# Kernel optimization log

Measured on AMD Instinct MI355X. Metric: run time of the kernel, lower is better.

## Reference

```python
import jax, jax.numpy as jnp
import numpy as np

B, S, D_IN = 2, 2048, 1024
H, DH = 16, 64          # num_heads, hidden_size (per-head dim)
D_MODEL = H * DH        # 1024
D_OUT = DH * 8          # 512


def setup_inputs() -> dict:
    key = jax.random.key(0)
    ks = jax.random.split(key, 9)
    s_in = 1.0 / np.sqrt(D_IN)
    s_md = 1.0 / np.sqrt(D_MODEL)
    return {
        "x": jax.random.normal(ks[0], (B, S, D_IN), dtype=jnp.float32),
        "Wq": jax.random.uniform(ks[1], (D_IN, D_MODEL), jnp.float32, -s_in, s_in),
        "bq": jax.random.uniform(ks[2], (D_MODEL,), jnp.float32, -s_in, s_in),
        "Wk": jax.random.uniform(ks[3], (D_IN, D_MODEL), jnp.float32, -s_in, s_in),
        "bk": jax.random.uniform(ks[4], (D_MODEL,), jnp.float32, -s_in, s_in),
        "Wv": jax.random.uniform(ks[5], (D_IN, D_MODEL), jnp.float32, -s_in, s_in),
        "bv": jax.random.uniform(ks[6], (D_MODEL,), jnp.float32, -s_in, s_in),
        "Wo": jax.random.uniform(ks[7], (D_MODEL, D_OUT), jnp.float32, -s_md, s_md),
        "bo": jax.random.uniform(ks[8], (D_OUT,), jnp.float32, -s_md, s_md),
    }


def reference(x, Wq, bq, Wk, bk, Wv, bv, Wo, bo):
    b, s, _ = x.shape
    # QKV projections -> [B, H, S, DH]
    def proj(W, bias):
        y = jnp.einsum("bsd,de->bse", x, W) + bias
        return y.reshape(b, s, H, DH).transpose(0, 2, 1, 3)
    Q, K, V = proj(Wq, bq), proj(Wk, bk), proj(Wv, bv)
    scores = jnp.einsum("bhqd,bhkd->bhqk", Q, K) / jnp.sqrt(jnp.float32(DH))
    weights = jax.nn.softmax(scores, axis=-1)
    attn = jnp.einsum("bhqk,bhkd->bhqd", weights, V)  # [B, H, S, DH]
    attn = attn.transpose(0, 2, 1, 3).reshape(b, s, H * DH)
    return jnp.einsum("bsd,de->bse", attn, Wo) + bo
```

## Files before the change

### kernel.cpp

```cpp
#include <hip/hip_runtime.h>

typedef __attribute__((ext_vector_type(8))) __bf16 bf16x8;
typedef __attribute__((ext_vector_type(4))) __bf16 bf16x4;
typedef __attribute__((ext_vector_type(4))) float f32x4;

#define MFMA16x16x32(A, B, C) __builtin_amdgcn_mfma_f32_16x16x32_bf16(A, B, C, 0, 0, 0)

__device__ __forceinline__ unsigned short f2bf(float f) {
    unsigned int u = __float_as_uint(f);
    u += 0x7fffu + ((u >> 16) & 1u);
    return (unsigned short)(u >> 16);
}

__device__ __forceinline__ unsigned cvtpk_bf16(float lo, float hi) {
    unsigned r;
    asm("v_cvt_pk_bf16_f32 %0, %1, %2" : "=v"(r) : "v"(lo), "v"(hi));
    return r;
}

__device__ __forceinline__ float exp2_hw(float x) {
    float r;
    asm("v_exp_f32 %0, %1" : "=v"(r) : "v"(x));
    return r;
}

__device__ __forceinline__ void gload16(const void* src, void* lds) {
    __builtin_amdgcn_global_load_lds(
        (const __attribute__((address_space(1))) unsigned int*)src,
        (__attribute__((address_space(3))) unsigned int*)lds,
        16, 0, 0);
}

__global__ __launch_bounds__(256) void cvt_x_kernel(const float* __restrict__ x,
                                                    unsigned short* __restrict__ xb) {
    const int i = (blockIdx.x * 256 + threadIdx.x) * 4;
    const float4 v = *(const float4*)(x + i);
    ushort4 o;
    o.x = f2bf(v.x); o.y = f2bf(v.y); o.z = f2bf(v.z); o.w = f2bf(v.w);
    *(ushort4*)(xb + i) = o;
}

__global__ __launch_bounds__(256) void tr_w_all_kernel(
    const float* __restrict__ Wq, const float* __restrict__ Wk,
    const float* __restrict__ Wv, const float* __restrict__ Wo,
    unsigned short* __restrict__ Wqt, unsigned short* __restrict__ Wkt,
    unsigned short* __restrict__ Wvt, unsigned short* __restrict__ Wot)
{
    __shared__ float tile[32][33];
    int y = blockIdx.y;
    const float* W; unsigned short* Wt; int N;
    if (y < 32)      { W = Wq; Wt = Wqt; N = 1024; }
    else if (y < 64) { W = Wk; Wt = Wkt; N = 1024; y -= 32; }
    else if (y < 96) { W = Wv; Wt = Wvt; N = 1024; y -= 64; }
    else             { W = Wo; Wt = Wot; N = 512;  y -= 96; }
    const int k0 = blockIdx.x * 32;
    const int n0 = y * 32;
    const int tx = threadIdx.x, ty = threadIdx.y;
#pragma unroll
    for (int i = 0; i < 4; ++i)
        tile[ty + 8 * i][tx] = W[(size_t)(k0 + ty + 8 * i) * N + n0 + tx];
    __syncthreads();
#pragma unroll
    for (int i = 0; i < 4; ++i)
        Wt[(size_t)(n0 + ty + 8 * i) * 1024 + k0 + tx] = f2bf(tile[tx][ty + 8 * i]);
}

__global__ __launch_bounds__(256, 3) void gemm_qkv_kernel(
    const unsigned short* __restrict__ xb,
    const unsigned short* __restrict__ Wqt,
    const unsigned short* __restrict__ Wkt,
    const unsigned short* __restrict__ Wvt,
    const float* __restrict__ bq, const float* __restrict__ bk, const float* __restrict__ bv,
    unsigned short* __restrict__ Qb, unsigned short* __restrict__ Kb, unsigned short* __restrict__ Vt)
{
    __shared__ unsigned short sA[2][128 * 32];
    __shared__ unsigned short sB[2][128 * 32];

    const int tid  = threadIdx.x;
    const int lane = tid & 63;
    const int w    = tid >> 6;
    const int wm   = w >> 1, wn = w & 1;
    const int li   = lane & 15, gg = lane >> 4;

    const int L  = blockIdx.y * 24 + blockIdx.x;
    const int v  = (L & 7) * 96 + (L >> 3);
    const int vx = v >> 5;
    const int vy = v & 31;
    const int m0    = vy * 128;
    const int which = vx >> 3;
    const int nloc0 = (vx & 7) * 128;

    const unsigned short* Wt = (which == 0) ? Wqt : ((which == 1) ? Wkt : Wvt);
    const float* bias        = (which == 0) ? bq  : ((which == 1) ? bk  : bv);
    const float osc          = (which == 0) ? 0.18033688011112042f : 1.0f;

    const int srow = lane >> 2;
    const int schk = lane & 3;

    f32x4 acc[4][4];
#pragma unroll
    for (int i = 0; i < 4; ++i)
#pragma unroll
        for (int j = 0; j < 4; ++j)
            acc[i][j] = (f32x4){0.f, 0.f, 0.f, 0.f};

    int aoff[4], boff[4];
#pragma unroll
    for (int f = 0; f < 4; ++f) {
        const int ra = wm * 64 + f * 16 + li;
        aoff[f] = ra * 32 + ((gg ^ ((ra >> 1) & 3)) * 8);
        const int rb = wn * 64 + f * 16 + li;
        boff[f] = rb * 32 + ((gg ^ ((rb >> 1) & 3)) * 8);
    }

#pragma unroll
    for (int j = 0; j < 2; ++j) {
        const int rl = (w * 2 + j) * 16 + srow;
        const int c  = schk ^ ((rl >> 1) & 3);
        gload16(xb + (size_t)(m0 + rl) * 1024 + c * 8,   sA[0] + (w * 2 + j) * 512);
        gload16(Wt + (size_t)(nloc0 + rl) * 1024 + c * 8, sB[0] + (w * 2 + j) * 512);
    }
    __syncthreads();

    for (int kt = 0; kt < 32; ++kt) {
        const int cur = kt & 1;
        if (kt < 31) {
            const int k1 = (kt + 1) * 32;
#pragma unroll
            for (int j = 0; j < 2; ++j) {
                const int rl = (w * 2 + j) * 16 + srow;
                const int c  = schk ^ ((rl >> 1) & 3);
                gload16(xb + (size_t)(m0 + rl) * 1024 + k1 + c * 8,   sA[cur ^ 1] + (w * 2 + j) * 512);
                gload16(Wt + (size_t)(nloc0 + rl) * 1024 + k1 + c * 8, sB[cur ^ 1] + (w * 2 + j) * 512);
            }
        }
        bf16x8 av[4], bw[4];
#pragma unroll
        for (int f = 0; f < 4; ++f) av[f] = *(const bf16x8*)(sA[cur] + aoff[f]);
#pragma unroll
        for (int f = 0; f < 4; ++f) bw[f] = *(const bf16x8*)(sB[cur] + boff[f]);
#pragma unroll
        for (int mf = 0; mf < 4; ++mf)
#pragma unroll
            for (int nf = 0; nf < 4; ++nf)
                acc[mf][nf] = MFMA16x16x32(av[mf], bw[nf], acc[mf][nf]);
        __syncthreads();
    }

    if (which == 2) {
#pragma unroll
        for (int nf = 0; nf < 4; ++nf) {
            const int nl = nloc0 + wn * 64 + nf * 16 + li;
            const float bi = bias[nl];
            const int h = nl >> 6, d = nl & 63;
#pragma unroll
            for (int mf = 0; mf < 4; ++mf) {
                const int m = m0 + wm * 64 + mf * 16 + gg * 4;
                const int b = m >> 11, s0 = m & 2047;
                ushort4 o;
                o.x = f2bf(acc[mf][nf][0] + bi);
                o.y = f2bf(acc[mf][nf][1] + bi);
                o.z = f2bf(acc[mf][nf][2] + bi);
                o.w = f2bf(acc[mf][nf][3] + bi);
                *(ushort4*)(Vt + (((size_t)(b * 16 + h)) * 64 + d) * 2048 + s0) = o;
            }
        }
    } else {
        unsigned short* dst = (which == 0) ? Qb : Kb;
#pragma unroll
        for (int nf = 0; nf < 4; ++nf) {
            const int nl = nloc0 + wn * 64 + nf * 16 + li;
            const float bi = bias[nl];
            const int h = nl >> 6, d = nl & 63;
#pragma unroll
            for (int mf = 0; mf < 4; ++mf) {
#pragma unroll
                for (int r = 0; r < 4; ++r) {
                    const int m = m0 + wm * 64 + mf * 16 + gg * 4 + r;
                    const int b = m >> 11, s = m & 2047;
                    dst[(((size_t)(b * 16 + h)) * 2048 + s) * 64 + d] = f2bf((acc[mf][nf][r] + bi) * osc);
                }
            }
        }
    }
}

__global__ __launch_bounds__(512, 4) void attn_kernel(
    const unsigned short* __restrict__ Qb,
    const unsigned short* __restrict__ Kb,
    const unsigned short* __restrict__ Vt,
    unsigned short* __restrict__ Ob)
{
    __shared__ unsigned short sK[2][64 * 64];
    __shared__ unsigned short sV[2][64 * 64];

    const int tid  = threadIdx.x;
    const int lane = tid & 63;
    const int w    = tid >> 6;
    const int li   = lane & 15, gg = lane >> 4;

    const int L  = blockIdx.y * 16 + blockIdx.x;
    const int v  = (L & 7) * 64 + (L >> 3);
    const int bh = v >> 4;
    const int q0 = (v & 15) * 128 + w * 16;

    const int slot = w * 64 + lane;
    const int srow = slot >> 3;
    const int schk = (slot & 7) ^ (srow & 7);

    const unsigned short* Kbase = Kb + ((size_t)bh * 2048 + srow) * 64 + schk * 8;
    const unsigned short* Vbase = Vt + ((size_t)bh * 64 + srow) * 2048 + schk * 8;

    bf16x8 qf[2];
#pragma unroll
    for (int kk = 0; kk < 2; ++kk) {
        const int q = q0 + li;
        const int d = kk * 32 + gg * 8;
        qf[kk] = *(const bf16x8*)(Qb + ((size_t)bh * 2048 + q) * 64 + d);
    }

    f32x4 acc[4];
#pragma unroll
    for (int df = 0; df < 4; ++df) acc[df] = (f32x4){0.f, 0.f, 0.f, 0.f};
    float l_s = 0.f;

    gload16(Kbase, sK[0] + slot * 8);
    gload16(Vbase, sV[0] + slot * 8);
    __syncthreads();

    for (int t = 0; t < 32; ++t) {
        const int cur = t & 1;
        if (t < 31) {
            gload16(Kbase + (size_t)(t + 1) * 4096, sK[cur ^ 1] + slot * 8);
            gload16(Vbase + (size_t)(t + 1) * 64,   sV[cur ^ 1] + slot * 8);
        }

        bf16x8 kf[4][2];
#pragma unroll
        for (int nf = 0; nf < 4; ++nf)
#pragma unroll
            for (int kk = 0; kk < 2; ++kk) {
                const int n = nf * 16 + li;
                const int ch = kk * 4 + gg;
                kf[nf][kk] = *(const bf16x8*)(sK[cur] + n * 64 + ((ch ^ (n & 7)) * 8));
            }
        f32x4 st[4];
        __builtin_amdgcn_s_setprio(1);
#pragma unroll
        for (int nf = 0; nf < 4; ++nf) {
            st[nf] = (f32x4){0.f, 0.f, 0.f, 0.f};
            st[nf] = MFMA16x16x32(kf[nf][0], qf[0], st[nf]);
            st[nf] = MFMA16x16x32(kf[nf][1], qf[1], st[nf]);
        }
        __builtin_amdgcn_s_setprio(0);

        float rs = 0.f;
        unsigned pk[4][2];
#pragma unroll
        for (int nf = 0; nf < 4; ++nf) {
#pragma unroll
            for (int r = 0; r < 4; ++r) {
                const float p = exp2_hw(st[nf][r]);
                st[nf][r] = p;
                rs += p;
            }
            pk[nf][0] = cvtpk_bf16(st[nf][0], st[nf][1]);
            pk[nf][1] = cvtpk_bf16(st[nf][2], st[nf][3]);
        }
        l_s += rs;

        bf16x8 pf[2];
#pragma unroll
        for (int kk = 0; kk < 2; ++kk) {
            unsigned A = pk[2 * kk][0], C = pk[2 * kk + 1][0];
            unsigned B = pk[2 * kk][1], D = pk[2 * kk + 1][1];
            asm("v_permlane32_swap_b32 %0, %1" : "+v"(A), "+v"(C));
            asm("v_permlane16_swap_b32 %0, %1" : "+v"(A), "+v"(C));
            asm("v_permlane32_swap_b32 %0, %1" : "+v"(B), "+v"(D));
            asm("v_permlane16_swap_b32 %0, %1" : "+v"(B), "+v"(D));
            uint4 u;
            u.x = A; u.y = B; u.z = C; u.w = D;
            pf[kk] = *reinterpret_cast<bf16x8*>(&u);
        }

        bf16x8 vf[4][2];
#pragma unroll
        for (int df = 0; df < 4; ++df)
#pragma unroll
            for (int kk = 0; kk < 2; ++kk) {
                const int n = df * 16 + li;
                const int ch = kk * 4 + gg;
                vf[df][kk] = *(const bf16x8*)(sV[cur] + n * 64 + ((ch ^ (n & 7)) * 8));
            }
        __builtin_amdgcn_s_setprio(1);
#pragma unroll
        for (int df = 0; df < 4; ++df) {
            acc[df] = MFMA16x16x32(pf[0], vf[df][0], acc[df]);
            acc[df] = MFMA16x16x32(pf[1], vf[df][1], acc[df]);
        }
        __builtin_amdgcn_s_setprio(0);
        __syncthreads();
    }

    float lf = l_s;
    lf += __shfl_xor(lf, 16, 64);
    lf += __shfl_xor(lf, 32, 64);

    const int b = bh >> 4, h = bh & 15;
#pragma unroll
    for (int r = 0; r < 4; ++r) {
        const float lbc = __shfl(lf, gg * 4 + r, 64);
        const float rl = 1.0f / lbc;
        const int q = q0 + gg * 4 + r;
#pragma unroll
        for (int df = 0; df < 4; ++df) {
            const int d = df * 16 + li;
            Ob[(((size_t)b * 2048 + q) * 16 + h) * 64 + d] = f2bf(acc[df][r] * rl);
        }
    }
}

__global__ __launch_bounds__(256, 2) void gemm_out_kernel(
    const unsigned short* __restrict__ attn,
    const unsigned short* __restrict__ Wot,
    const float* __restrict__ bo,
    float* __restrict__ out)
{
    __shared__ unsigned short sA[2][64 * 32];
    __shared__ unsigned short sB[2][128 * 32];

    const int tid  = threadIdx.x;
    const int lane = tid & 63;
    const int w    = tid >> 6;
    const int wm   = w >> 1, wn = w & 1;
    const int li   = lane & 15, gg = lane >> 4;
    const int m0   = blockIdx.y * 64;
    const int n0   = blockIdx.x * 128;

    const int arow = tid >> 2;
    const int acol = tid & 3;

    f32x4 acc[2][4];
#pragma unroll
    for (int i = 0; i < 2; ++i)
#pragma unroll
        for (int j = 0; j < 4; ++j)
            acc[i][j] = (f32x4){0.f, 0.f, 0.f, 0.f};

    int aoff[2], boff[4];
#pragma unroll
    for (int f = 0; f < 2; ++f) {
        const int ra = wm * 32 + f * 16 + li;
        aoff[f] = ra * 32 + ((gg ^ ((ra >> 1) & 3)) * 8);
    }
#pragma unroll
    for (int f = 0; f < 4; ++f) {
        const int rb = wn * 64 + f * 16 + li;
        boff[f] = rb * 32 + ((gg ^ ((rb >> 1) & 3)) * 8);
    }

    {
        const int ca = acol ^ ((arow >> 1) & 3);
        gload16(attn + (size_t)(m0 + arow) * 1024 + ca * 8, sA[0] + tid * 8);
#pragma unroll
        for (int jj = 0; jj < 2; ++jj) {
            const int rb = jj * 64 + arow;
            const int cb = acol ^ ((rb >> 1) & 3);
            gload16(Wot + (size_t)(n0 + rb) * 1024 + cb * 8, sB[0] + (jj * 256 + tid) * 8);
        }
    }
    __syncthreads();

    for (int kt = 0; kt < 32; ++kt) {
        const int cur = kt & 1;
        if (kt < 31) {
            const int k1 = (kt + 1) * 32;
            const int ca = acol ^ ((arow >> 1) & 3);
            gload16(attn + (size_t)(m0 + arow) * 1024 + k1 + ca * 8, sA[cur ^ 1] + tid * 8);
#pragma unroll
            for (int jj = 0; jj < 2; ++jj) {
                const int rb = jj * 64 + arow;
                const int cb = acol ^ ((rb >> 1) & 3);
                gload16(Wot + (size_t)(n0 + rb) * 1024 + k1 + cb * 8, sB[cur ^ 1] + (jj * 256 + tid) * 8);
            }
        }
        bf16x8 av[2], bw[4];
#pragma unroll
        for (int f = 0; f < 2; ++f) av[f] = *(const bf16x8*)(sA[cur] + aoff[f]);
#pragma unroll
        for (int f = 0; f < 4; ++f) bw[f] = *(const bf16x8*)(sB[cur] + boff[f]);
#pragma unroll
        for (int mf = 0; mf < 2; ++mf)
#pragma unroll
            for (int nf = 0; nf < 4; ++nf)
                acc[mf][nf] = MFMA16x16x32(av[mf], bw[nf], acc[mf][nf]);
        __syncthreads();
    }

#pragma unroll
    for (int nf = 0; nf < 4; ++nf) {
        const int n = n0 + wn * 64 + nf * 16 + li;
        const float bi = bo[n];
#pragma unroll
        for (int mf = 0; mf < 2; ++mf) {
#pragma unroll
            for (int r = 0; r < 4; ++r) {
                const int m = m0 + wm * 32 + mf * 16 + gg * 4 + r;
                out[(size_t)m * 512 + n] = acc[mf][nf][r] + bi;
            }
        }
    }
}

extern "C" void kernel_launch(void* const* d_in, const int* in_sizes, int n_in,
                              void* d_out, int out_size, void* d_ws, size_t ws_size,
                              hipStream_t stream) {
    const float* x  = (const float*)d_in[0];
    const float* Wq = (const float*)d_in[1];
    const float* bq = (const float*)d_in[2];
    const float* Wk = (const float*)d_in[3];
    const float* bk = (const float*)d_in[4];
    const float* Wv = (const float*)d_in[5];
    const float* bv = (const float*)d_in[6];
    const float* Wo = (const float*)d_in[7];
    const float* bo = (const float*)d_in[8];
    float* out = (float*)d_out;

    unsigned short* ws  = (unsigned short*)d_ws;
    unsigned short* xb  = ws;
    unsigned short* Wqt = xb  + 4194304;
    unsigned short* Wkt = Wqt + 1048576;
    unsigned short* Wvt = Wkt + 1048576;
    unsigned short* Wot = Wvt + 1048576;
    unsigned short* Qb  = Wot + 524288;
    unsigned short* Kb  = Qb  + 4194304;
    unsigned short* Vt  = Kb  + 4194304;
    unsigned short* attnb = Vt + 4194304;

    cvt_x_kernel<<<dim3(4096), dim3(256), 0, stream>>>(x, xb);
    tr_w_all_kernel<<<dim3(32, 112), dim3(32, 8), 0, stream>>>(Wq, Wk, Wv, Wo,
                                                               Wqt, Wkt, Wvt, Wot);
    gemm_qkv_kernel<<<dim3(24, 32), dim3(256), 0, stream>>>(xb, Wqt, Wkt, Wvt,
                                                            bq, bk, bv, Qb, Kb, Vt);
    attn_kernel<<<dim3(16, 32), dim3(512), 0, stream>>>(Qb, Kb, Vt, attnb);
    gemm_out_kernel<<<dim3(4, 64), dim3(256), 0, stream>>>(attnb, Wot, bo, out);
}
```

Before: 110.3 us.

## Process two query tiles per wave in attention, halving block size to 256

```diff
diff --git a/kernel.cpp b/kernel.cpp
--- a/kernel.cpp
+++ b/kernel.cpp
@@ -185,7 +185,7 @@
     }
 }
 
-__global__ __launch_bounds__(512, 4) void attn_kernel(
+__global__ __launch_bounds__(256, 4) void attn_kernel(
     const unsigned short* __restrict__ Qb,
     const unsigned short* __restrict__ Kb,
     const unsigned short* __restrict__ Vt,
@@ -202,37 +202,49 @@
     const int L  = blockIdx.y * 16 + blockIdx.x;
     const int v  = (L & 7) * 64 + (L >> 3);
     const int bh = v >> 4;
-    const int q0 = (v & 15) * 128 + w * 16;
-
-    const int slot = w * 64 + lane;
-    const int srow = slot >> 3;
-    const int schk = (slot & 7) ^ (srow & 7);
-
-    const unsigned short* Kbase = Kb + ((size_t)bh * 2048 + srow) * 64 + schk * 8;
-    const unsigned short* Vbase = Vt + ((size_t)bh * 64 + srow) * 2048 + schk * 8;
-
-    bf16x8 qf[2];
-#pragma unroll
-    for (int kk = 0; kk < 2; ++kk) {
-        const int q = q0 + li;
-        const int d = kk * 32 + gg * 8;
-        qf[kk] = *(const bf16x8*)(Qb + ((size_t)bh * 2048 + q) * 64 + d);
-    }
-
-    f32x4 acc[4];
-#pragma unroll
-    for (int df = 0; df < 4; ++df) acc[df] = (f32x4){0.f, 0.f, 0.f, 0.f};
-    float l_s = 0.f;
-
-    gload16(Kbase, sK[0] + slot * 8);
-    gload16(Vbase, sV[0] + slot * 8);
+    const int q0 = (v & 15) * 128 + w * 32;
+
+    const int slot0 = w * 64 + lane;
+    const int srow0 = slot0 >> 3;
+    const int sch0  = (slot0 & 7) ^ (srow0 & 7);
+
+    const unsigned short* Kbase = Kb + ((size_t)bh * 2048 + srow0) * 64 + sch0 * 8;
+    const unsigned short* Vbase = Vt + ((size_t)bh * 64 + srow0) * 2048 + sch0 * 8;
+
+    bf16x8 qf[2][2];
+#pragma unroll
+    for (int mq = 0; mq < 2; ++mq)
+#pragma unroll
+        for (int kk = 0; kk < 2; ++kk) {
+            const int q = q0 + mq * 16 + li;
+            const int d = kk * 32 + gg * 8;
+            qf[mq][kk] = *(const bf16x8*)(Qb + ((size_t)bh * 2048 + q) * 64 + d);
+        }
+
+    f32x4 acc[2][4];
+    float l_s[2];
+#pragma unroll
+    for (int mq = 0; mq < 2; ++mq) {
+#pragma unroll
+        for (int df = 0; df < 4; ++df) acc[mq][df] = (f32x4){0.f, 0.f, 0.f, 0.f};
+        l_s[mq] = 0.f;
+    }
+
+    gload16(Kbase,               sK[0] + slot0 * 8);
+    gload16(Kbase + 32 * 64,     sK[0] + slot0 * 8 + 2048);
+    gload16(Vbase,               sV[0] + slot0 * 8);
+    gload16(Vbase + 32 * 2048,   sV[0] + slot0 * 8 + 2048);
     __syncthreads();
 
     for (int t = 0; t < 32; ++t) {
         const int cur = t & 1;
         if (t < 31) {
-            gload16(Kbase + (size_t)(t + 1) * 4096, sK[cur ^ 1] + slot * 8);
-            gload16(Vbase + (size_t)(t + 1) * 64,   sV[cur ^ 1] + slot * 8);
+            const size_t ko = (size_t)(t + 1) * 4096;
+            const size_t vo = (size_t)(t + 1) * 64;
+            gload16(Kbase + ko,             sK[cur ^ 1] + slot0 * 8);
+            gload16(Kbase + ko + 32 * 64,   sK[cur ^ 1] + slot0 * 8 + 2048);
+            gload16(Vbase + vo,             sV[cur ^ 1] + slot0 * 8);
+            gload16(Vbase + vo + 32 * 2048, sV[cur ^ 1] + slot0 * 8 + 2048);
         }
 
         bf16x8 kf[4][2];
@@ -244,43 +256,47 @@
                 const int ch = kk * 4 + gg;
                 kf[nf][kk] = *(const bf16x8*)(sK[cur] + n * 64 + ((ch ^ (n & 7)) * 8));
             }
-        f32x4 st[4];
-        __builtin_amdgcn_s_setprio(1);
-#pragma unroll
-        for (int nf = 0; nf < 4; ++nf) {
-            st[nf] = (f32x4){0.f, 0.f, 0.f, 0.f};
-            st[nf] = MFMA16x16x32(kf[nf][0], qf[0], st[nf]);
-            st[nf] = MFMA16x16x32(kf[nf][1], qf[1], st[nf]);
-        }
-        __builtin_amdgcn_s_setprio(0);
-
-        float rs = 0.f;
-        unsigned pk[4][2];
-#pragma unroll
-        for (int nf = 0; nf < 4; ++nf) {
-#pragma unroll
-            for (int r = 0; r < 4; ++r) {
-                const float p = exp2_hw(st[nf][r]);
-                st[nf][r] = p;
-                rs += p;
-            }
-            pk[nf][0] = cvtpk_bf16(st[nf][0], st[nf][1]);
-            pk[nf][1] = cvtpk_bf16(st[nf][2], st[nf][3]);
-        }
-        l_s += rs;
-
-        bf16x8 pf[2];
-#pragma unroll
-        for (int kk = 0; kk < 2; ++kk) {
-            unsigned A = pk[2 * kk][0], C = pk[2 * kk + 1][0];
-            unsigned B = pk[2 * kk][1], D = pk[2 * kk + 1][1];
-            asm("v_permlane32_swap_b32 %0, %1" : "+v"(A), "+v"(C));
-            asm("v_permlane16_swap_b32 %0, %1" : "+v"(A), "+v"(C));
-            asm("v_permlane32_swap_b32 %0, %1" : "+v"(B), "+v"(D));
-            asm("v_permlane16_swap_b32 %0, %1" : "+v"(B), "+v"(D));
-            uint4 u;
-            u.x = A; u.y = B; u.z = C; u.w = D;
-            pf[kk] = *reinterpret_cast<bf16x8*>(&u);
+
+        bf16x8 pf[2][2];
+#pragma unroll
+        for (int mq = 0; mq < 2; ++mq) {
+            f32x4 st[4];
+            __builtin_amdgcn_s_setprio(1);
+#pragma unroll
+            for (int nf = 0; nf < 4; ++nf) {
+                st[nf] = (f32x4){0.f, 0.f, 0.f, 0.f};
+                st[nf] = MFMA16x16x32(kf[nf][0], qf[mq][0], st[nf]);
+                st[nf] = MFMA16x16x32(kf[nf][1], qf[mq][1], st[nf]);
+            }
+            __builtin_amdgcn_s_setprio(0);
+
+            float rs = 0.f;
+            unsigned pk[4][2];
+#pragma unroll
+            for (int nf = 0; nf < 4; ++nf) {
+#pragma unroll
+                for (int r = 0; r < 4; ++r) {
+                    const float p = exp2_hw(st[nf][r]);
+                    st[nf][r] = p;
+                    rs += p;
+                }
+                pk[nf][0] = cvtpk_bf16(st[nf][0], st[nf][1]);
+                pk[nf][1] = cvtpk_bf16(st[nf][2], st[nf][3]);
+            }
+            l_s[mq] += rs;
+
+#pragma unroll
+            for (int kk = 0; kk < 2; ++kk) {
+                unsigned A = pk[2 * kk][0], C = pk[2 * kk + 1][0];
+                unsigned B = pk[2 * kk][1], D = pk[2 * kk + 1][1];
+                asm("v_permlane32_swap_b32 %0, %1" : "+v"(A), "+v"(C));
+                asm("v_permlane16_swap_b32 %0, %1" : "+v"(A), "+v"(C));
+                asm("v_permlane32_swap_b32 %0, %1" : "+v"(B), "+v"(D));
+                asm("v_permlane16_swap_b32 %0, %1" : "+v"(B), "+v"(D));
+                uint4 u;
+                u.x = A; u.y = B; u.z = C; u.w = D;
+                pf[mq][kk] = *reinterpret_cast<bf16x8*>(&u);
+            }
         }
 
         bf16x8 vf[4][2];
@@ -294,28 +310,32 @@
             }
         __builtin_amdgcn_s_setprio(1);
 #pragma unroll
-        for (int df = 0; df < 4; ++df) {
-            acc[df] = MFMA16x16x32(pf[0], vf[df][0], acc[df]);
-            acc[df] = MFMA16x16x32(pf[1], vf[df][1], acc[df]);
-        }
+        for (int mq = 0; mq < 2; ++mq)
+#pragma unroll
+            for (int df = 0; df < 4; ++df) {
+                acc[mq][df] = MFMA16x16x32(pf[mq][0], vf[df][0], acc[mq][df]);
+                acc[mq][df] = MFMA16x16x32(pf[mq][1], vf[df][1], acc[mq][df]);
+            }
         __builtin_amdgcn_s_setprio(0);
         __syncthreads();
     }
 
-    float lf = l_s;
-    lf += __shfl_xor(lf, 16, 64);
-    lf += __shfl_xor(lf, 32, 64);
-
     const int b = bh >> 4, h = bh & 15;
 #pragma unroll
-    for (int r = 0; r < 4; ++r) {
-        const float lbc = __shfl(lf, gg * 4 + r, 64);
-        const float rl = 1.0f / lbc;
-        const int q = q0 + gg * 4 + r;
-#pragma unroll
-        for (int df = 0; df < 4; ++df) {
-            const int d = df * 16 + li;
-            Ob[(((size_t)b * 2048 + q) * 16 + h) * 64 + d] = f2bf(acc[df][r] * rl);
+    for (int mq = 0; mq < 2; ++mq) {
+        float lf = l_s[mq];
+        lf += __shfl_xor(lf, 16, 64);
+        lf += __shfl_xor(lf, 32, 64);
+#pragma unroll
+        for (int r = 0; r < 4; ++r) {
+            const float lbc = __shfl(lf, gg * 4 + r, 64);
+            const float rl = 1.0f / lbc;
+            const int q = q0 + mq * 16 + gg * 4 + r;
+#pragma unroll
+            for (int df = 0; df < 4; ++df) {
+                const int d = df * 16 + li;
+                Ob[(((size_t)b * 2048 + q) * 16 + h) * 64 + d] = f2bf(acc[mq][df][r] * rl);
+            }
         }
     }
 }
@@ -442,6 +462,6 @@
                                                                Wqt, Wkt, Wvt, Wot);
     gemm_qkv_kernel<<<dim3(24, 32), dim3(256), 0, stream>>>(xb, Wqt, Wkt, Wvt,
                                                             bq, bk, bv, Qb, Kb, Vt);
-    attn_kernel<<<dim3(16, 32), dim3(512), 0, stream>>>(Qb, Kb, Vt, attnb);
+    attn_kernel<<<dim3(16, 32), dim3(256), 0, stream>>>(Qb, Kb, Vt, attnb);
     gemm_out_kernel<<<dim3(4, 64), dim3(256), 0, stream>>>(attnb, Wot, bo, out);
 }
```

Result: slower. 143.4 us (+30.0%).
